# Kernel tuning notes

Hardware: AMD Instinct MI355X
Metric: run time of the kernel (lower is better)

## Reference

```python
import jax, jax.numpy as jnp
import numpy as np

DIM = 128
EXPAND = 2
INTERNAL = DIM * EXPAND  # 256
MAX_SEQ = 2048
BATCH = 32
GATE_DECAY = 3.0


def _gated_cell(x, Wa, ba, Wi, bi, g):
    # x: [B,S,D]; Wa,Wi: [E,D]; ba,bi,g: [E]
    pa = jnp.einsum('bsd,ed->bse', x, Wa) + ba          # projected activation
    pi = jnp.einsum('bsd,ed->bse', x, Wi) + bi          # projected input
    reset_gate = jax.nn.sigmoid(pa)
    input_gate = jax.nn.sigmoid(pi)
    alpha = jax.nn.sigmoid(g)                           # [E]
    a = alpha / jnp.power(GATE_DECAY, reset_gate)       # adaptive alpha [B,S,E]
    u = jnp.sqrt(1.0 - a * a) * (input_gate * pi)       # per-step input [B,S,E]

    def step(h, au):
        a_t, u_t = au
        h = a_t * h + u_t
        return h, h

    h0 = jnp.zeros((x.shape[0], Wa.shape[0]), x.dtype)
    _, ys = jax.lax.scan(step, h0, (a.transpose(1, 0, 2), u.transpose(1, 0, 2)))
    return ys.transpose(1, 0, 2)                        # [B,S,E]


def _recency_weights(seq_len, dtype):
    w = jnp.exp(jnp.linspace(0.0, 3.0, MAX_SEQ))[:seq_len]
    return w.astype(dtype).reshape(1, -1, 1)


def setup_inputs() -> dict:
    key = jax.random.key(0)
    ks = jax.random.split(key, 12)
    std = 1.0 / np.sqrt(DIM)  # kaiming fan_in linear
    lo = float(np.log(0.9 / 0.1))
    hi = float(np.log(0.999 / 0.001))
    d = {
        'x': jax.random.normal(ks[0], (BATCH, MAX_SEQ, DIM), jnp.float32),
        'Wa_u': jax.random.normal(ks[1], (INTERNAL, DIM), jnp.float32) * std,
        'ba_u': jnp.zeros((INTERNAL,), jnp.float32),
        'Wi_u': jax.random.normal(ks[2], (INTERNAL, DIM), jnp.float32) * std,
        'bi_u': jnp.zeros((INTERNAL,), jnp.float32),
        'g_u': jax.random.uniform(ks[3], (INTERNAL,), jnp.float32, lo, hi),
        'Wa_w': jax.random.normal(ks[4], (INTERNAL, DIM), jnp.float32) * std,
        'ba_w': jnp.zeros((INTERNAL,), jnp.float32),
        'Wi_w': jax.random.normal(ks[5], (INTERNAL, DIM), jnp.float32) * std,
        'bi_w': jnp.zeros((INTERNAL,), jnp.float32),
        'g_w': jax.random.uniform(ks[6], (INTERNAL,), jnp.float32, lo, hi),
        'Wf': jax.random.normal(ks[7], (DIM, 4 * DIM), jnp.float32) * (1.0 / np.sqrt(4 * DIM)),
        'bf': jnp.zeros((DIM,), jnp.float32),
    }
    return d


def reference(x, Wa_u, ba_u, Wi_u, bi_u, g_u, Wa_w, ba_w, Wi_w, bi_w, g_w, Wf, bf):
    unweighted = _gated_cell(x, Wa_u, ba_u, Wi_u, bi_u, g_u)          # [B,S,2D]
    xw = x * _recency_weights(x.shape[1], x.dtype)
    weighted = _gated_cell(xw, Wa_w, ba_w, Wi_w, bi_w, g_w)           # [B,S,2D]
    combined = jnp.concatenate([unweighted, weighted], axis=-1)       # [B,S,4D]
    return jnp.einsum('bsf,df->bsd', combined, Wf) + bf               # [B,S,D]
```

## Files before the change

### kernel.cpp

```cpp
#include <hip/hip_runtime.h>
#include <hip/hip_fp16.h>
#include <cstddef>
#include <cstdint>

#define DIM 128
#define SEQ 2048
#define NB 32
#define NCH 512
#define NROWS (NB * SEQ)

typedef _Float16 half8 __attribute__((ext_vector_type(8)));
typedef float    f32x4 __attribute__((ext_vector_type(4)));

#define CMB_BYTES ((size_t)NROWS * NCH * 2)
#define WFG_OFF   CMB_BYTES
#define WFG_BYTES ((size_t)NCH * DIM * 2)
#define WS_NEEDED (WFG_OFF + WFG_BYTES)

__device__ __forceinline__ float sigf(float v) {
    return __builtin_amdgcn_rcpf(1.0f + __builtin_amdgcn_exp2f(v * -1.44269504f));
}

__device__ __forceinline__ half8 cvt8(float4 v0, float4 v1) {
    auto p0 = __builtin_amdgcn_cvt_pkrtz(v0.x, v0.y);
    auto p1 = __builtin_amdgcn_cvt_pkrtz(v0.z, v0.w);
    auto p2 = __builtin_amdgcn_cvt_pkrtz(v1.x, v1.y);
    auto p3 = __builtin_amdgcn_cvt_pkrtz(v1.z, v1.w);
    union U { half8 h8; decltype(p0) p[4]; } u;
    u.p[0] = p0; u.p[1] = p1; u.p[2] = p2; u.p[3] = p3;
    return u.h8;
}

__device__ __forceinline__ void gload_lds16(const _Float16* g, _Float16* l) {
    __builtin_amdgcn_global_load_lds(
        (const __attribute__((address_space(1))) void*)g,
        (__attribute__((address_space(3))) void*)l,
        16, 0, 0);
}

__global__ void k0_wfg(const float* __restrict__ Wf, _Float16* __restrict__ Wfg) {
    int t = blockIdx.x * 256 + threadIdx.x;
#pragma unroll
    for (int i = 0; i < 8; ++i) {
        int o = t * 8 + i;
        int j    = o & 7;
        int lane = (o >> 3) & 63;
        int q    = lane >> 4, n16 = lane & 15;
        int ct   = (o >> 9) & 7;
        int ks   = (o >> 12) & 1;
        int kb   = o >> 13;
        int k = kb * 64 + ks * 32 + q * 8 + j;
        int n = ct * 16 + n16;
        Wfg[o] = (_Float16)Wf[n * NCH + k];
    }
}

__global__ __launch_bounds__(512, 2) void kfused(
        const float* __restrict__ x,
        const float* __restrict__ Wa_u, const float* __restrict__ ba_u,
        const float* __restrict__ Wi_u, const float* __restrict__ bi_u,
        const float* __restrict__ g_u,
        const float* __restrict__ Wa_w, const float* __restrict__ ba_w,
        const float* __restrict__ Wi_w, const float* __restrict__ bi_w,
        const float* __restrict__ g_w,
        _Float16* __restrict__ cmb) {
    __shared__ _Float16 Bs[8192];
    __shared__ float2   Wseg[2][8][33];
    __shared__ float    carryL[2][32];

    const int tid  = threadIdx.x;
    const int lane = tid & 63;
    const int w    = tid >> 6;
    const int quad = lane >> 4;
    const int n16  = lane & 15;

    const int b  = blockIdx.x;
    const int cg = blockIdx.y;
    const int p  = cg >> 3;
    const int ebase = (cg & 7) * 32;

    const float* Wa  = p ? Wa_w : Wa_u;
    const float* Wi  = p ? Wi_w : Wi_u;
    const float* bap = p ? ba_w : ba_u;
    const float* bip = p ? bi_w : bi_u;
    const float* gp  = p ? g_w  : g_u;

    for (int sl = tid; sl < 1024; sl += 512) {
        int l  = sl & 63;
        int nt = (sl >> 6) & 3;
        int ks = sl >> 8;
        int qq = l >> 4, nn = l & 15;
        int e = ebase + (nt & 1) * 16 + nn;
        const float* Wp = (nt >> 1) ? Wi : Wa;
        const float* src = Wp + (size_t)e * DIM + ks * 32 + qq * 8;
        float4 v0 = *(const float4*)src;
        float4 v1 = *(const float4*)(src + 4);
        *(half8*)&Bs[sl * 8] = cvt8(v0, v1);
    }

    float rba[2], rbi[2], ral[2];
#pragma unroll
    for (int hh = 0; hh < 2; ++hh) {
        int e = ebase + hh * 16 + n16;
        rba[hh] = bap[e];
        rbi[hh] = bip[e];
        ral[hh] = sigf(gp[e]);
    }
    if (tid < 32) carryL[0][tid] = 0.0f;

    float scb = __expf((float)(w * 16 + quad * 4) * (3.0f / 2047.0f));
    const float r1    = __expf(3.0f / 2047.0f);
    const float r2    = r1 * r1;
    const float r3    = r2 * r1;
    const float cs128 = __expf(128.0f * 3.0f / 2047.0f);

    const float* xbase = x + ((size_t)b * SEQ + (size_t)(w * 16 + n16)) * DIM + quad * 8;
    _Float16* dst0 = cmb + (size_t)(cg >> 1) * 8192 + (size_t)w * 1024
                   + (size_t)(cg & 1) * 512
                   + (size_t)quad * 32 + (size_t)(n16 >> 3) * 128 + (n16 & 7);

    __syncthreads();

    half8 af[4];
    {
        float4 xf0[8];
#pragma unroll
        for (int ks = 0; ks < 4; ++ks) {
            xf0[2 * ks]     = *(const float4*)(xbase + ks * 32);
            xf0[2 * ks + 1] = *(const float4*)(xbase + ks * 32 + 4);
        }
#pragma unroll
        for (int ks = 0; ks < 4; ++ks)
            af[ks] = cvt8(xf0[2 * ks], xf0[2 * ks + 1]);
    }

    for (int t = 0; t < 16; ++t) {
        f32x4 acc[4];
#pragma unroll
        for (int nt = 0; nt < 4; ++nt) acc[nt] = (f32x4){0.f, 0.f, 0.f, 0.f};
#pragma unroll
        for (int ks = 0; ks < 4; ++ks) {
            half8 a = af[ks];
#pragma unroll
            for (int nt = 0; nt < 4; ++nt) {
                half8 bb = *(const half8*)&Bs[(ks * 256 + nt * 64 + lane) * 8];
                acc[nt] = __builtin_amdgcn_mfma_f32_16x16x32_f16(a, bb, acc[nt], 0, 0, 0);
            }
        }

        float4 xf[8];
        {
            int tn = (t + 1) & 15;
            const float* ab = xbase + (size_t)tn * 128 * DIM;
#pragma unroll
            for (int ks = 0; ks < 4; ++ks) {
                xf[2 * ks]     = *(const float4*)(ab + ks * 32);
                xf[2 * ks + 1] = *(const float4*)(ab + ks * 32 + 4);
            }
        }

        float sc[4];
        if (p) { sc[0] = scb; sc[1] = scb * r1; sc[2] = scb * r2; sc[3] = scb * r3; }
        else   { sc[0] = sc[1] = sc[2] = sc[3] = 1.0f; }
        scb *= cs128;

        float a_s[2][4], u_s[2][4];
        float IA[2], IU[2], EA[2], EU[2];
#pragma unroll
        for (int hh = 0; hh < 2; ++hh) {
            float A4 = 1.0f, U4 = 0.0f;
#pragma unroll
            for (int reg = 0; reg < 4; ++reg) {
                float pa = fmaf(acc[hh][reg],     sc[reg], rba[hh]);
                float pi = fmaf(acc[2 + hh][reg], sc[reg], rbi[hh]);
                float rst = sigf(pa);
                float ig  = sigf(pi);
                float a   = ral[hh] * __builtin_amdgcn_exp2f(-rst * 1.5849625007211562f);
                float m   = fmaxf(fmaf(-a, a, 1.0f), 0.0f);
                float u   = __builtin_amdgcn_sqrtf(m) * (ig * pi);
                a_s[hh][reg] = a; u_s[hh][reg] = u;
                A4 *= a;
                U4 = fmaf(a, U4, u);
            }
            float A = A4, U = U4;
            float Ap = __shfl_up(A, 16); float Up = __shfl_up(U, 16);
            bool c1 = quad >= 1;
            U = c1 ? fmaf(A, Up, U) : U;
            A = c1 ? A * Ap : A;
            Ap = __shfl_up(A, 32); Up = __shfl_up(U, 32);
            bool c2 = quad >= 2;
            U = c2 ? fmaf(A, Up, U) : U;
            A = c2 ? A * Ap : A;
            IA[hh] = A; IU[hh] = U;
            float Ae = __shfl_up(A, 16), Ue = __shfl_up(U, 16);
            EA[hh] = (quad == 0) ? 1.0f : Ae;
            EU[hh] = (quad == 0) ? 0.0f : Ue;
        }
        if (quad == 3) {
#pragma unroll
            for (int hh = 0; hh < 2; ++hh)
                Wseg[t & 1][w][hh * 16 + n16] = make_float2(IA[hh], IU[hh]);
        }

        __syncthreads();

#pragma unroll
        for (int ks = 0; ks < 4; ++ks)
            af[ks] = cvt8(xf[2 * ks], xf[2 * ks + 1]);

        _Float16* dstT = dst0 + (size_t)((b * 16 + t) * 8) * 8192;
#pragma unroll
        for (int hh = 0; hh < 2; ++hh) {
            int ch = hh * 16 + n16;
            float h = carryL[t & 1][ch];
#pragma unroll
            for (int jj = 0; jj < 7; ++jj) {
                if (jj < w) {
                    float2 v = Wseg[t & 1][jj][ch];
                    h = fmaf(v.x, h, v.y);
                }
            }
            h = fmaf(EA[hh], h, EU[hh]);
#pragma unroll
            for (int reg = 0; reg < 4; ++reg) {
                h = fmaf(a_s[hh][reg], h, u_s[hh][reg]);
                dstT[hh * 256 + reg * 8] = (_Float16)h;
            }
            if (w == 7 && quad == 3)
                carryL[(t + 1) & 1][ch] = h;
        }
    }
}

__global__ __launch_bounds__(256, 2) void k3_mfma(
        const _Float16* __restrict__ cmbF, const _Float16* __restrict__ Wfg,
        const float* __restrict__ bfv, float* __restrict__ out) {
    __shared__ _Float16 As[2][8192];
    __shared__ _Float16 Bs[2][8192];

    const int tid  = threadIdx.x;
    const int lane = tid & 63;
    const int w    = tid >> 6;
    const int rb   = blockIdx.x;
    const int row0 = rb * 128;
    const int q    = lane >> 4;
    const int nn   = lane & 15;

    f32x4 acc[2][8];
#pragma unroll
    for (int rt = 0; rt < 2; ++rt)
#pragma unroll
        for (int ct = 0; ct < 8; ++ct)
            acc[rt][ct] = (f32x4){0.0f, 0.0f, 0.0f, 0.0f};

#define K3_STAGE(buf, kb)                                                     \
    {                                                                         \
        const _Float16* sa = cmbF + ((size_t)rb * 8 + (kb)) * 8192            \
                           + (size_t)w * 2048 + (size_t)lane * 8;             \
        const _Float16* sb = Wfg + (size_t)(kb) * 8192                        \
                           + (size_t)w * 2048 + (size_t)lane * 8;             \
        _Float16* la = &As[buf][w * 2048];                                    \
        _Float16* lb = &Bs[buf][w * 2048];                                    \
        _Pragma("unroll")                                                     \
        for (int i = 0; i < 4; ++i) {                                         \
            gload_lds16(sa + i * 512, la + i * 512);                          \
            gload_lds16(sb + i * 512, lb + i * 512);                          \
        }                                                                     \
    }

    K3_STAGE(0, 0);
    __syncthreads();

    for (int kb = 0; kb < 8; ++kb) {
        const int cur = kb & 1;
        if (kb < 7) K3_STAGE(cur ^ 1, kb + 1);

#pragma unroll
        for (int ks = 0; ks < 2; ++ks) {
            half8 a0 = *(const half8*)&As[cur][(((w * 2 + 0) * 2 + ks) * 512) + lane * 8];
            half8 a1 = *(const half8*)&As[cur][(((w * 2 + 1) * 2 + ks) * 512) + lane * 8];
#pragma unroll
            for (int ct = 0; ct < 8; ++ct) {
                half8 bb = *(const half8*)&Bs[cur][((ks * 8 + ct) * 512) + lane * 8];
                acc[0][ct] = __builtin_amdgcn_mfma_f32_16x16x32_f16(a0, bb, acc[0][ct], 0, 0, 0);
                acc[1][ct] = __builtin_amdgcn_mfma_f32_16x16x32_f16(a1, bb, acc[1][ct], 0, 0, 0);
            }
        }
        __syncthreads();
    }

#pragma unroll
    for (int rt = 0; rt < 2; ++rt) {
        int rbase = row0 + w * 32 + rt * 16 + q * 4;
#pragma unroll
        for (int ct = 0; ct < 8; ++ct) {
            int col = ct * 16 + nn;
            float bias = bfv[col];
#pragma unroll
            for (int reg = 0; reg < 4; ++reg)
                out[(size_t)(rbase + reg) * DIM + col] = acc[rt][ct][reg] + bias;
        }
    }
#undef K3_STAGE
}

extern "C" void kernel_launch(void* const* d_in, const int* in_sizes, int n_in,
                              void* d_out, int out_size, void* d_ws, size_t ws_size,
                              hipStream_t stream) {
    if (ws_size < WS_NEEDED) return;

    const float* x    = (const float*)d_in[0];
    const float* Wa_u = (const float*)d_in[1];
    const float* ba_u = (const float*)d_in[2];
    const float* Wi_u = (const float*)d_in[3];
    const float* bi_u = (const float*)d_in[4];
    const float* g_u  = (const float*)d_in[5];
    const float* Wa_w = (const float*)d_in[6];
    const float* ba_w = (const float*)d_in[7];
    const float* Wi_w = (const float*)d_in[8];
    const float* bi_w = (const float*)d_in[9];
    const float* g_w  = (const float*)d_in[10];
    const float* Wf   = (const float*)d_in[11];
    const float* bfv  = (const float*)d_in[12];
    float* out = (float*)d_out;

    char* ws = (char*)d_ws;
    _Float16* cmb = (_Float16*)ws;
    _Float16* Wfg = (_Float16*)(ws + WFG_OFF);

    hipLaunchKernelGGL(k0_wfg, dim3(32), dim3(256), 0, stream, Wf, Wfg);
    hipLaunchKernelGGL(kfused, dim3(32, 16), dim3(512), 0, stream,
                       x, Wa_u, ba_u, Wi_u, bi_u, g_u,
                       Wa_w, ba_w, Wi_w, bi_w, g_w, cmb);
    hipLaunchKernelGGL(k3_mfma, dim3(512), dim3(256), 0, stream,
                       cmb, Wfg, bfv, out);
}
```

Before: 189.4 us.

## Halve channels per block in fused scan kernel and remap grid for XCD locality

The fused projection+scan kernel now handles 16 channels per block instead of 32, doubling the grid to 1024 blocks and raising the launch-bounds occupancy hint to 8. Blocks are linearized so that the blocks for a given batch land on the same XCD, which is meant to improve L2 reuse of x. The sigmoid for the reset gate folds the log2e scaling into the bias and scale constants. The aim is more parallelism and latency hiding. In exchange, x is reloaded by twice as many blocks and the per-block MFMA work shrinks.

Result: slower. 257.1 us (+35.7%).

```diff
diff --git a/kernel.cpp b/kernel.cpp
--- a/kernel.cpp
+++ b/kernel.cpp
@@ -55,7 +55,7 @@
     }
 }
 
-__global__ __launch_bounds__(512, 2) void kfused(
+__global__ __launch_bounds__(512, 8) void kfused(
         const float* __restrict__ x,
         const float* __restrict__ Wa_u, const float* __restrict__ ba_u,
         const float* __restrict__ Wi_u, const float* __restrict__ bi_u,
@@ -64,9 +64,9 @@
         const float* __restrict__ Wi_w, const float* __restrict__ bi_w,
         const float* __restrict__ g_w,
         _Float16* __restrict__ cmb) {
-    __shared__ _Float16 Bs[8192];
-    __shared__ float2   Wseg[2][8][33];
-    __shared__ float    carryL[2][32];
+    __shared__ _Float16 Bs[4096];
+    __shared__ float2   Wseg[2][8][17];
+    __shared__ float    carryL[2][16];
 
     const int tid  = threadIdx.x;
     const int lane = tid & 63;
@@ -74,10 +74,14 @@
     const int quad = lane >> 4;
     const int n16  = lane & 15;
 
-    const int b  = blockIdx.x;
-    const int cg = blockIdx.y;
-    const int p  = cg >> 3;
-    const int ebase = (cg & 7) * 32;
+    const int lin = blockIdx.x;
+    const int xcd = lin & 7;
+    const int idx = lin >> 3;
+    const int b   = xcd * 4 + (idx & 3);
+    const int cg  = idx >> 2;
+    const int p   = cg >> 4;
+    const int cgl = cg & 15;
+    const int ebase = cgl * 16;
 
     const float* Wa  = p ? Wa_w : Wa_u;
     const float* Wi  = p ? Wi_w : Wi_u;
@@ -85,28 +89,30 @@
     const float* bip = p ? bi_w : bi_u;
     const float* gp  = p ? g_w  : g_u;
 
-    for (int sl = tid; sl < 1024; sl += 512) {
+    {
+        int sl = tid;
         int l  = sl & 63;
-        int nt = (sl >> 6) & 3;
-        int ks = sl >> 8;
+        int nt = (sl >> 6) & 1;
+        int ks = sl >> 7;
         int qq = l >> 4, nn = l & 15;
-        int e = ebase + (nt & 1) * 16 + nn;
-        const float* Wp = (nt >> 1) ? Wi : Wa;
+        int e = ebase + nn;
+        const float* Wp = nt ? Wi : Wa;
         const float* src = Wp + (size_t)e * DIM + ks * 32 + qq * 8;
         float4 v0 = *(const float4*)src;
         float4 v1 = *(const float4*)(src + 4);
         *(half8*)&Bs[sl * 8] = cvt8(v0, v1);
     }
 
-    float rba[2], rbi[2], ral[2];
-#pragma unroll
-    for (int hh = 0; hh < 2; ++hh) {
-        int e = ebase + hh * 16 + n16;
-        rba[hh] = bap[e];
-        rbi[hh] = bip[e];
-        ral[hh] = sigf(gp[e]);
-    }
-    if (tid < 32) carryL[0][tid] = 0.0f;
+    const float NL2E = -1.44269504f;
+    float rba, rbi, ral, rba2;
+    {
+        int e = ebase + n16;
+        rba = bap[e];
+        rbi = bip[e];
+        ral = sigf(gp[e]);
+        rba2 = rba * NL2E;
+    }
+    if (tid < 16) carryL[0][tid] = 0.0f;
 
     float scb = __expf((float)(w * 16 + quad * 4) * (3.0f / 2047.0f));
     const float r1    = __expf(3.0f / 2047.0f);
@@ -115,9 +121,11 @@
     const float cs128 = __expf(128.0f * 3.0f / 2047.0f);
 
     const float* xbase = x + ((size_t)b * SEQ + (size_t)(w * 16 + n16)) * DIM + quad * 8;
-    _Float16* dst0 = cmb + (size_t)(cg >> 1) * 8192 + (size_t)w * 1024
-                   + (size_t)(cg & 1) * 512
-                   + (size_t)quad * 32 + (size_t)(n16 >> 3) * 128 + (n16 & 7);
+    const int kbp = p * 4 + (cgl >> 2);
+    _Float16* dst0 = cmb + (size_t)kbp * 8192 + (size_t)w * 1024
+                   + (size_t)((cgl >> 1) & 1) * 512
+                   + (size_t)((cgl & 1) * 2 + (n16 >> 3)) * 128
+                   + (size_t)quad * 32 + (n16 & 7);
 
     __syncthreads();
 
@@ -135,15 +143,15 @@
     }
 
     for (int t = 0; t < 16; ++t) {
-        f32x4 acc[4];
-#pragma unroll
-        for (int nt = 0; nt < 4; ++nt) acc[nt] = (f32x4){0.f, 0.f, 0.f, 0.f};
+        f32x4 acc[2];
+#pragma unroll
+        for (int nt = 0; nt < 2; ++nt) acc[nt] = (f32x4){0.f, 0.f, 0.f, 0.f};
 #pragma unroll
         for (int ks = 0; ks < 4; ++ks) {
             half8 a = af[ks];
 #pragma unroll
-            for (int nt = 0; nt < 4; ++nt) {
-                half8 bb = *(const half8*)&Bs[(ks * 256 + nt * 64 + lane) * 8];
+            for (int nt = 0; nt < 2; ++nt) {
+                half8 bb = *(const half8*)&Bs[(ks * 128 + nt * 64 + lane) * 8];
                 acc[nt] = __builtin_amdgcn_mfma_f32_16x16x32_f16(a, bb, acc[nt], 0, 0, 0);
             }
         }
@@ -159,26 +167,27 @@
             }
         }
 
-        float sc[4];
+        float sc[4], sc2[4];
         if (p) { sc[0] = scb; sc[1] = scb * r1; sc[2] = scb * r2; sc[3] = scb * r3; }
         else   { sc[0] = sc[1] = sc[2] = sc[3] = 1.0f; }
         scb *= cs128;
-
-        float a_s[2][4], u_s[2][4];
-        float IA[2], IU[2], EA[2], EU[2];
-#pragma unroll
-        for (int hh = 0; hh < 2; ++hh) {
+#pragma unroll
+        for (int reg = 0; reg < 4; ++reg) sc2[reg] = sc[reg] * NL2E;
+
+        float a_s[4], u_s[4];
+        float IA, IU, EAx, EUx;
+        {
             float A4 = 1.0f, U4 = 0.0f;
 #pragma unroll
             for (int reg = 0; reg < 4; ++reg) {
-                float pa = fmaf(acc[hh][reg],     sc[reg], rba[hh]);
-                float pi = fmaf(acc[2 + hh][reg], sc[reg], rbi[hh]);
-                float rst = sigf(pa);
+                float pi  = fmaf(acc[1][reg], sc[reg], rbi);
+                float ea  = __builtin_amdgcn_exp2f(fmaf(acc[0][reg], sc2[reg], rba2));
+                float rst = __builtin_amdgcn_rcpf(1.0f + ea);
                 float ig  = sigf(pi);
-                float a   = ral[hh] * __builtin_amdgcn_exp2f(-rst * 1.5849625007211562f);
+                float a   = ral * __builtin_amdgcn_exp2f(-rst * 1.5849625007211562f);
                 float m   = fmaxf(fmaf(-a, a, 1.0f), 0.0f);
                 float u   = __builtin_amdgcn_sqrtf(m) * (ig * pi);
-                a_s[hh][reg] = a; u_s[hh][reg] = u;
+                a_s[reg] = a; u_s[reg] = u;
                 A4 *= a;
                 U4 = fmaf(a, U4, u);
             }
@@ -191,16 +200,13 @@
             bool c2 = quad >= 2;
             U = c2 ? fmaf(A, Up, U) : U;
             A = c2 ? A * Ap : A;
-            IA[hh] = A; IU[hh] = U;
+            IA = A; IU = U;
             float Ae = __shfl_up(A, 16), Ue = __shfl_up(U, 16);
-            EA[hh] = (quad == 0) ? 1.0f : Ae;
-            EU[hh] = (quad == 0) ? 0.0f : Ue;
-        }
-        if (quad == 3) {
-#pragma unroll
-            for (int hh = 0; hh < 2; ++hh)
-                Wseg[t & 1][w][hh * 16 + n16] = make_float2(IA[hh], IU[hh]);
-        }
+            EAx = (quad == 0) ? 1.0f : Ae;
+            EUx = (quad == 0) ? 0.0f : Ue;
+        }
+        if (quad == 3)
+            Wseg[t & 1][w][n16] = make_float2(IA, IU);
 
         __syncthreads();
 
@@ -209,25 +215,23 @@
             af[ks] = cvt8(xf[2 * ks], xf[2 * ks + 1]);
 
         _Float16* dstT = dst0 + (size_t)((b * 16 + t) * 8) * 8192;
-#pragma unroll
-        for (int hh = 0; hh < 2; ++hh) {
-            int ch = hh * 16 + n16;
-            float h = carryL[t & 1][ch];
+        {
+            float h = carryL[t & 1][n16];
 #pragma unroll
             for (int jj = 0; jj < 7; ++jj) {
                 if (jj < w) {
-                    float2 v = Wseg[t & 1][jj][ch];
+                    float2 v = Wseg[t & 1][jj][n16];
                     h = fmaf(v.x, h, v.y);
                 }
             }
-            h = fmaf(EA[hh], h, EU[hh]);
+            h = fmaf(EAx, h, EUx);
 #pragma unroll
             for (int reg = 0; reg < 4; ++reg) {
-                h = fmaf(a_s[hh][reg], h, u_s[hh][reg]);
-                dstT[hh * 256 + reg * 8] = (_Float16)h;
+                h = fmaf(a_s[reg], h, u_s[reg]);
+                dstT[reg * 8] = (_Float16)h;
             }
             if (w == 7 && quad == 3)
-                carryL[(t + 1) & 1][ch] = h;
+                carryL[(t + 1) & 1][n16] = h;
         }
     }
 }
@@ -329,7 +333,7 @@
     _Float16* Wfg = (_Float16*)(ws + WFG_OFF);
 
     hipLaunchKernelGGL(k0_wfg, dim3(32), dim3(256), 0, stream, Wf, Wfg);
-    hipLaunchKernelGGL(kfused, dim3(32, 16), dim3(512), 0, stream,
+    hipLaunchKernelGGL(kfused, dim3(1024), dim3(512), 0, stream,
                        x, Wa_u, ba_u, Wi_u, bi_u, g_u,
                        Wa_w, ba_w, Wi_w, bi_w, g_w, cmb);
     hipLaunchKernelGGL(k3_mfma, dim3(512), dim3(256), 0, stream,
```
